# Kernel optimization log

Measured on AMD Instinct MI355X. Metric: run time of the kernel, lower is better.

The kernel has to match this reference:

```python
import jax, jax.numpy as jnp
import numpy as np

B, T, D = 64, 512, 1024
V_TAG, V_TYPE = 6, 20
TAG_PAD, TYPE_PAD = 5, 19
E = 2048          # total entity spans in the batch (sliced cascade mode)
MAX_SPAN = 8      # max entity span length


def setup_inputs() -> dict:
    key = jax.random.key(0)
    ks = jax.random.split(key, 12)
    full_hidden = jax.random.normal(ks[0], (B, T, D), dtype=jnp.float32)
    W_tag = jax.random.normal(ks[1], (D, V_TAG), dtype=jnp.float32) * 0.02
    b_tag = jnp.zeros((V_TAG,), jnp.float32)
    W_type = jax.random.normal(ks[2], (D, V_TYPE), dtype=jnp.float32) * 0.02
    b_type = jnp.zeros((V_TYPE,), jnp.float32)
    crf_start = jax.random.normal(ks[3], (V_TAG,), dtype=jnp.float32) * 0.1
    crf_end = jax.random.normal(ks[4], (V_TAG,), dtype=jnp.float32) * 0.1
    crf_trans = jax.random.normal(ks[5], (V_TAG, V_TAG), dtype=jnp.float32) * 0.1
    # ragged sequence lengths (>= MAX_SPAN+1 so all positions/spans are sane)
    seq_lens = jnp.maximum(jax.random.randint(ks[6], (B,), 1, T + 1), MAX_SPAN + 1).astype(jnp.int32)
    tag_ids = jax.random.randint(ks[7], (B, T), 0, V_TAG - 1).astype(jnp.int32)  # exclude pad tag
    ent_sample_ids = jax.random.randint(ks[8], (E,), 0, B).astype(jnp.int32)
    ent_starts = jax.random.randint(ks[9], (E,), 0, T - MAX_SPAN).astype(jnp.int32)
    ent_lens = jax.random.randint(ks[10], (E,), 1, MAX_SPAN + 1)
    ent_ends = (ent_starts + ent_lens).astype(jnp.int32)
    ent_type_ids = jax.random.randint(ks[11], (E,), 0, V_TYPE - 1).astype(jnp.int32)  # exclude pad type
    return dict(full_hidden=full_hidden, W_tag=W_tag, b_tag=b_tag, W_type=W_type,
                b_type=b_type, crf_start=crf_start, crf_end=crf_end, crf_trans=crf_trans,
                tag_ids=tag_ids, seq_lens=seq_lens, ent_sample_ids=ent_sample_ids,
                ent_starts=ent_starts, ent_ends=ent_ends, ent_type_ids=ent_type_ids)


def reference(full_hidden, W_tag, b_tag, W_type, b_type, crf_start, crf_end, crf_trans,
              tag_ids, seq_lens, ent_sample_ids, ent_starts, ent_ends, ent_type_ids):
    mask = jnp.arange(T)[None, :] < seq_lens[:, None]                  # [B,T] bool (tok_mask)
    maskf = mask.astype(full_hidden.dtype)

    # ---- base CRF decoder: tag projection + CRF NLL per sample ----
    tag_feats = full_hidden @ W_tag + b_tag                            # [B,T,V_TAG]

    # gold path score
    emit_scores = jnp.take_along_axis(tag_feats, tag_ids[..., None].astype(jnp.int32), axis=-1)[..., 0]  # [B,T]
    gold = crf_start[tag_ids[:, 0]] + jnp.sum(emit_scores * maskf, axis=1)
    trans_scores = crf_trans[tag_ids[:, :-1], tag_ids[:, 1:]]          # [B,T-1]
    gold = gold + jnp.sum(trans_scores * maskf[:, 1:], axis=1)
    last_tags = tag_ids[jnp.arange(B), seq_lens - 1]
    gold = gold + crf_end[last_tags]

    # log-partition via forward algorithm (log-sum-exp DP, lax.scan over time)
    alpha0 = crf_start[None, :] + tag_feats[:, 0]                      # [B,V]

    def step(alpha, xs):
        emit_t, mask_t = xs                                            # [B,V], [B]
        new = jax.scipy.special.logsumexp(
            alpha[:, :, None] + crf_trans[None, :, :] + emit_t[:, None, :], axis=1)
        return jnp.where(mask_t[:, None], new, alpha), None

    alphaT, _ = jax.lax.scan(step, alpha0,
                             (jnp.swapaxes(tag_feats, 0, 1)[1:], mask.T[1:]))
    logZ = jax.scipy.special.logsumexp(alphaT + crf_end[None, :], axis=-1)  # [B]
    tag_losses = logZ - gold                                           # per-sample CRF NLL

    # ---- sliced cascade: entity-span mean pooling + CE(sum) per sample ----
    type_feats = full_hidden @ W_type + b_type                         # [B,T,V_TYPE]
    csum = jnp.pad(jnp.cumsum(type_feats, axis=1), ((0, 0), (1, 0), (0, 0)))  # [B,T+1,V_TYPE]
    span_sum = csum[ent_sample_ids, ent_ends] - csum[ent_sample_ids, ent_starts]  # [E,V_TYPE]
    span_len = (ent_ends - ent_starts).astype(type_feats.dtype)
    ent_feats = span_sum / span_len[:, None]                           # mean over span
    logp = jax.nn.log_softmax(ent_feats, axis=-1)
    ent_ce = -jnp.take_along_axis(logp, ent_type_ids[:, None].astype(jnp.int32), axis=-1)[:, 0]
    valid = (ent_type_ids != TYPE_PAD).astype(ent_ce.dtype)            # ignore_index
    type_losses = jax.ops.segment_sum(ent_ce * valid, ent_sample_ids, num_segments=B)
    return tag_losses + type_losses                                    # [B]
```

## Files before the change

kernel.cpp:

```cpp
#include <hip/hip_runtime.h>
#include <math.h>
#include <stdint.h>

#define NB  64
#define NT  512
#define ND  1024
#define NVT 6
#define NVY 20
#define TYPE_PAD_V 19
#define NE  2048
#define LOG2E 1.44269504088896340736f
#define LN2   0.69314718055994530942f

typedef float v2f __attribute__((ext_vector_type(2)));

#define OFF_WTT 196608
#define OFF_CNT 217088
#define OFF_WS2 217104

__global__ __launch_bounds__(256) void k1_tagfeats(const float* __restrict__ H,
                                                   const float* __restrict__ W_tag,
                                                   const float* __restrict__ b_tag,
                                                   const float* __restrict__ W_type,
                                                   float* __restrict__ ws,
                                                   float* __restrict__ out) {
    float* featsT = ws;
    float* WtT    = ws + OFF_WTT;
    if (blockIdx.x == 0) {
        if (threadIdx.x < NB) out[threadIdx.x] = 0.0f;
        if (threadIdx.x == 64) ((int*)(ws + OFF_CNT))[0] = 0;
    }
    if (blockIdx.x < 32) {
        int tid = blockIdx.x * 256 + threadIdx.x;
        for (int i = tid; i < NVY * ND; i += 32 * 256)
            WtT[i] = W_type[(i & (ND - 1)) * NVY + (i >> 10)];
    }

    __shared__ float wlds[NVT][ND];
    for (int i = threadIdx.x; i < ND * NVT; i += 256) {
        int d = i / NVT, v = i % NVT;
        wlds[v][d] = W_tag[i];
    }
    __syncthreads();
    float bt[NVT];
#pragma unroll
    for (int v = 0; v < NVT; ++v) bt[v] = b_tag[v];

    const int lane = threadIdx.x & 63;
    const int wid  = threadIdx.x >> 6;
    const int qw   = lane >> 4;
    const int ql   = lane & 15;
    const int rowBase = blockIdx.x * 32;

#pragma unroll
    for (int it = 0; it < 2; ++it) {
        const int r = rowBase + it * 16 + wid * 4 + qw;
        const float4* hrow = (const float4*)(H + (size_t)r * ND);
        float acc[NVT] = {0.f, 0.f, 0.f, 0.f, 0.f, 0.f};
#pragma unroll
        for (int k = 0; k < 16; ++k) {
            float4 h = hrow[ql + 16 * k];
#pragma unroll
            for (int v = 0; v < NVT; ++v) {
                float4 w = ((const float4*)&wlds[v][0])[ql + 16 * k];
                acc[v] += h.x * w.x + h.y * w.y + h.z * w.z + h.w * w.w;
            }
        }
#pragma unroll
        for (int v = 0; v < NVT; ++v) {
#pragma unroll
            for (int off = 8; off >= 1; off >>= 1)
                acc[v] += __shfl_xor(acc[v], off);
        }
        const int bb = r >> 9;
        const int tt = r & (NT - 1);
#pragma unroll
        for (int v = 0; v < NVT; ++v)
            if (ql == v) featsT[(size_t)tt * 384 + bb * 6 + v] = acc[v] + bt[v];
    }
}

#define LOADC(BUF, c) do {                                                   \
    _Pragma("unroll")                                                        \
    for (int kk = 0; kk < 6; ++kk) {                                         \
        const float4* p = src4 + (size_t)((c) * 6 + kk) * 128;               \
        BUF[2 * kk] = p[0]; BUF[2 * kk + 1] = p[1];                          \
    }                                                                        \
} while (0)

#define CBODY(BUF, c) do {                                                   \
    float i0 = BUF[1].z, i1 = BUF[3].z, i2 = BUF[5].z,                       \
          i3 = BUF[7].z, i4 = BUF[9].z, i5 = BUF[11].z;                      \
    float im = fmaxf(fmaxf(fmaxf(i0, i1), i2), fmaxf(fmaxf(i3, i4), i5));    \
    float w0 = q0 * __builtin_amdgcn_exp2f(i0 - im);                         \
    float w1 = q1 * __builtin_amdgcn_exp2f(i1 - im);                         \
    float w2 = q2 * __builtin_amdgcn_exp2f(i2 - im);                         \
    float w3 = q3 * __builtin_amdgcn_exp2f(i3 - im);                         \
    float w4 = q4 * __builtin_amdgcn_exp2f(i4 - im);                         \
    float w5 = q5 * __builtin_amdgcn_exp2f(i5 - im);                         \
    float n0 = BUF[0].x * w0, n1 = BUF[0].y * w0, n2 = BUF[0].z * w0,        \
          n3 = BUF[0].w * w0, n4 = BUF[1].x * w0, n5 = BUF[1].y * w0;        \
    n0 = __builtin_fmaf(BUF[2].x,  w1, n0); n1 = __builtin_fmaf(BUF[2].y,  w1, n1); \
    n2 = __builtin_fmaf(BUF[2].z,  w1, n2); n3 = __builtin_fmaf(BUF[2].w,  w1, n3); \
    n4 = __builtin_fmaf(BUF[3].x,  w1, n4); n5 = __builtin_fmaf(BUF[3].y,  w1, n5); \
    n0 = __builtin_fmaf(BUF[4].x,  w2, n0); n1 = __builtin_fmaf(BUF[4].y,  w2, n1); \
    n2 = __builtin_fmaf(BUF[4].z,  w2, n2); n3 = __builtin_fmaf(BUF[4].w,  w2, n3); \
    n4 = __builtin_fmaf(BUF[5].x,  w2, n4); n5 = __builtin_fmaf(BUF[5].y,  w2, n5); \
    n0 = __builtin_fmaf(BUF[6].x,  w3, n0); n1 = __builtin_fmaf(BUF[6].y,  w3, n1); \
    n2 = __builtin_fmaf(BUF[6].z,  w3, n2); n3 = __builtin_fmaf(BUF[6].w,  w3, n3); \
    n4 = __builtin_fmaf(BUF[7].x,  w3, n4); n5 = __builtin_fmaf(BUF[7].y,  w3, n5); \
    n0 = __builtin_fmaf(BUF[8].x,  w4, n0); n1 = __builtin_fmaf(BUF[8].y,  w4, n1); \
    n2 = __builtin_fmaf(BUF[8].z,  w4, n2); n3 = __builtin_fmaf(BUF[8].w,  w4, n3); \
    n4 = __builtin_fmaf(BUF[9].x,  w4, n4); n5 = __builtin_fmaf(BUF[9].y,  w4, n5); \
    n0 = __builtin_fmaf(BUF[10].x, w5, n0); n1 = __builtin_fmaf(BUF[10].y, w5, n1); \
    n2 = __builtin_fmaf(BUF[10].z, w5, n2); n3 = __builtin_fmaf(BUF[10].w, w5, n3); \
    n4 = __builtin_fmaf(BUF[11].x, w5, n4); n5 = __builtin_fmaf(BUF[11].y, w5, n5); \
    float qmax = fmaxf(fmaxf(fmaxf(n0, n1), n2), fmaxf(fmaxf(n3, n4), n5));  \
    uint32_t eb = __float_as_uint(qmax) >> 23;                               \
    mAcc2 += (float)((int)eb - 126) + im;                                    \
    float ri = __uint_as_float((uint32_t)(253 - eb) << 23);                  \
    q0 = n0 * ri; q1 = n1 * ri; q2 = n2 * ri;                                \
    q3 = n3 * ri; q4 = n4 * ri; q5 = n5 * ri;                                \
    int lc = (c) + 3; if (lc > 31) lc = 31;                                  \
    LOADC(BUF, lc);                                                          \
} while (0)

__global__ __launch_bounds__(64) void k2_fused(
    const float* __restrict__ H,
    const float* __restrict__ b_type,
    const float* __restrict__ crf_start,
    const float* __restrict__ crf_end,
    const float* __restrict__ crf_trans,
    const int* __restrict__ tag_ids,
    const int* __restrict__ seq_lens,
    const int* __restrict__ ent_sid,
    const int* __restrict__ ent_st,
    const int* __restrict__ ent_en,
    const int* __restrict__ ent_ty,
    float* __restrict__ ws,
    float* __restrict__ out) {
    const float* featsT = ws;
    const float* WtT    = ws + OFF_WTT;
    int* cnt            = (int*)(ws + OFF_CNT);
    float* ws2          = ws + OFF_WS2;
    __shared__ int stag[NT];
    __shared__ float trLp[NVT * NVT];
    __shared__ int isLast;
    const int lane = threadIdx.x;

    if (blockIdx.x < 192) {
        const int c = blockIdx.x / 6;
        const int k = blockIdx.x - 6 * c;
        const int b = lane;
        const int L = seq_lens[b];
        float F[NVT][NVT];
#pragma unroll
        for (int i = 0; i < NVT; ++i)
#pragma unroll
            for (int j = 0; j < NVT; ++j)
                F[i][j] = __builtin_amdgcn_exp2f(crf_trans[i * NVT + j] * LOG2E);
        const char* pf = (const char*)featsT + b * 24;
        v2f Ebuf[16][3];
#pragma unroll
        for (int u = 0; u < 16; ++u) {
            const v2f* p = (const v2f*)(pf + (size_t)(16 * c + 1 + u) * 1536);
            Ebuf[u][0] = p[0]; Ebuf[u][1] = p[1]; Ebuf[u][2] = p[2];
        }
        float v0, v1, v2, v3, v4, v5;
        v0 = (k == 0) ? 1.f : 0.f; v1 = (k == 1) ? 1.f : 0.f; v2 = (k == 2) ? 1.f : 0.f;
        v3 = (k == 3) ? 1.f : 0.f; v4 = (k == 4) ? 1.f : 0.f; v5 = (k == 5) ? 1.f : 0.f;
        int isc = 0;
#pragma unroll
        for (int u = 0; u < 16; ++u) {
            float e0 = __builtin_amdgcn_exp2f(Ebuf[u][0].x * LOG2E);
            float e1 = __builtin_amdgcn_exp2f(Ebuf[u][0].y * LOG2E);
            float e2 = __builtin_amdgcn_exp2f(Ebuf[u][1].x * LOG2E);
            float e3 = __builtin_amdgcn_exp2f(Ebuf[u][1].y * LOG2E);
            float e4 = __builtin_amdgcn_exp2f(Ebuf[u][2].x * LOG2E);
            float e5 = __builtin_amdgcn_exp2f(Ebuf[u][2].y * LOG2E);
            bool ok = (16 * c + 1 + u) < L;
            float g[NVT];
#pragma unroll
            for (int j = 0; j < NVT; ++j) {
                float s = F[0][j] * v0;
                s = __builtin_fmaf(F[1][j], v1, s);
                s = __builtin_fmaf(F[2][j], v2, s);
                s = __builtin_fmaf(F[3][j], v3, s);
                s = __builtin_fmaf(F[4][j], v4, s);
                s = __builtin_fmaf(F[5][j], v5, s);
                g[j] = s;
            }
            v0 = ok ? e0 * g[0] : v0;  v1 = ok ? e1 * g[1] : v1;
            v2 = ok ? e2 * g[2] : v2;  v3 = ok ? e3 * g[3] : v3;
            v4 = ok ? e4 * g[4] : v4;  v5 = ok ? e5 * g[5] : v5;
            if ((u & 3) == 3) {
                float qmax = fmaxf(fmaxf(fmaxf(v0, v1), v2), fmaxf(fmaxf(v3, v4), v5));
                uint32_t eb = __float_as_uint(qmax) >> 23;
                float ri = __uint_as_float((uint32_t)(253 - eb) << 23);
                v0 *= ri; v1 *= ri; v2 *= ri; v3 *= ri; v4 *= ri; v5 *= ri;
                isc += (int)eb - 126;
            }
        }
        float4* dst = (float4*)(ws2 + (((size_t)c * 6 + k) * 64 + b) * 8);
        dst[0] = make_float4(v0, v1, v2, v3);
        dst[1] = make_float4(v4, v5, (float)isc, 0.0f);

        __threadfence();
        if (lane == 0) isLast = (atomicAdd(cnt, 1) == 191);
        __syncthreads();
        if (isLast) {
            __threadfence();
            const int b2 = lane;
            float a0[NVT];
#pragma unroll
            for (int j = 0; j < NVT; ++j) a0[j] = crf_start[j] + featsT[b2 * 6 + j];
            float m0 = fmaxf(fmaxf(fmaxf(a0[0], a0[1]), a0[2]),
                             fmaxf(fmaxf(a0[3], a0[4]), a0[5]));
            float q0 = __builtin_amdgcn_exp2f((a0[0] - m0) * LOG2E);
            float q1 = __builtin_amdgcn_exp2f((a0[1] - m0) * LOG2E);
            float q2 = __builtin_amdgcn_exp2f((a0[2] - m0) * LOG2E);
            float q3 = __builtin_amdgcn_exp2f((a0[3] - m0) * LOG2E);
            float q4 = __builtin_amdgcn_exp2f((a0[4] - m0) * LOG2E);
            float q5 = __builtin_amdgcn_exp2f((a0[5] - m0) * LOG2E);
            float mAcc2 = m0 * LOG2E;

            const float4* src4 = (const float4*)ws2 + b2 * 2;
            float4 PB0[12], PB1[12], PB2[12];
            LOADC(PB0, 0); LOADC(PB1, 1); LOADC(PB2, 2);
#pragma unroll 1
            for (int c0 = 0; c0 < 30; c0 += 3) {
                CBODY(PB0, c0);
                CBODY(PB1, c0 + 1);
                CBODY(PB2, c0 + 2);
            }
            CBODY(PB0, 30);
            CBODY(PB1, 31);

            float zs = q0 * __builtin_amdgcn_exp2f(crf_end[0] * LOG2E)
                     + q1 * __builtin_amdgcn_exp2f(crf_end[1] * LOG2E)
                     + q2 * __builtin_amdgcn_exp2f(crf_end[2] * LOG2E)
                     + q3 * __builtin_amdgcn_exp2f(crf_end[3] * LOG2E)
                     + q4 * __builtin_amdgcn_exp2f(crf_end[4] * LOG2E)
                     + q5 * __builtin_amdgcn_exp2f(crf_end[5] * LOG2E);
            float logZ = LN2 * (mAcc2 + __builtin_amdgcn_logf(zs));
            atomicAdd(&out[b2], logZ);
        }
    } else if (blockIdx.x < 192 + NB) {
        const int b = blockIdx.x - 192;
        for (int i = lane; i < NT; i += 64) stag[i] = tag_ids[b * NT + i];
        if (lane < NVT * NVT) trLp[lane] = crf_trans[lane];
        __syncthreads();
        const int L = seq_lens[b];
        float g = 0.0f;
#pragma unroll
        for (int k = 0; k < NT / 64; ++k) {
            int t = lane + 64 * k;
            if (t < L) {
                int tg = stag[t];
                g += featsT[(size_t)t * 384 + b * 6 + tg];
                if (t >= 1) g += trLp[stag[t - 1] * NVT + tg];
            }
        }
#pragma unroll
        for (int off = 32; off >= 1; off >>= 1) g += __shfl_xor(g, off);
        if (lane == 0)
            atomicAdd(&out[b], -(g + crf_start[stag[0]] + crf_end[stag[L - 1]]));
    } else {
        const int e  = blockIdx.x - 192 - NB;
        const int bb = ent_sid[e];
        const int s  = ent_st[e];
        const int en = ent_en[e];
        const int ty = ent_ty[e];
        float4 sv[4];
#pragma unroll
        for (int k = 0; k < 4; ++k) { sv[k].x = 0.f; sv[k].y = 0.f; sv[k].z = 0.f; sv[k].w = 0.f; }
        for (int t = s; t < en; ++t) {
            const float4* hr = (const float4*)(H + ((size_t)bb * NT + t) * ND);
#pragma unroll
            for (int k = 0; k < 4; ++k) {
                float4 h = hr[lane + 64 * k];
                sv[k].x += h.x; sv[k].y += h.y; sv[k].z += h.z; sv[k].w += h.w;
            }
        }
        const float inv = 1.0f / (float)(en - s);
        float f[NVY];
#pragma unroll
        for (int v = 0; v < NVY; ++v) {
            const float4* wv = (const float4*)(WtT + v * ND);
            float p = 0.0f;
#pragma unroll
            for (int k = 0; k < 4; ++k) {
                float4 w = wv[lane + 64 * k];
                p += sv[k].x * w.x + sv[k].y * w.y + sv[k].z * w.z + sv[k].w * w.w;
            }
#pragma unroll
            for (int off = 32; off >= 1; off >>= 1) p += __shfl_xor(p, off);
            f[v] = p * inv + b_type[v];
        }
        float mx = -3.0e38f;
#pragma unroll
        for (int v = 0; v < NVY; ++v) mx = fmaxf(mx, f[v]);
        float sum = 0.0f, goldf = 0.0f;
#pragma unroll
        for (int v = 0; v < NVY; ++v) {
            sum += __expf(f[v] - mx);
            if (v == ty) goldf = f[v];
        }
        float lse = mx + __logf(sum);
        if (ty != TYPE_PAD_V && lane == 0) atomicAdd(&out[bb], lse - goldf);
    }
}

extern "C" void kernel_launch(void* const* d_in, const int* in_sizes, int n_in,
                              void* d_out, int out_size, void* d_ws, size_t ws_size,
                              hipStream_t stream) {
    const float* H         = (const float*)d_in[0];
    const float* W_tag     = (const float*)d_in[1];
    const float* b_tag     = (const float*)d_in[2];
    const float* W_type    = (const float*)d_in[3];
    const float* b_type    = (const float*)d_in[4];
    const float* crf_start = (const float*)d_in[5];
    const float* crf_end   = (const float*)d_in[6];
    const float* crf_trans = (const float*)d_in[7];
    const int* tag_ids     = (const int*)d_in[8];
    const int* seq_lens    = (const int*)d_in[9];
    const int* ent_sid     = (const int*)d_in[10];
    const int* ent_st      = (const int*)d_in[11];
    const int* ent_en      = (const int*)d_in[12];
    const int* ent_ty      = (const int*)d_in[13];
    float* out = (float*)d_out;
    float* ws  = (float*)d_ws;

    hipLaunchKernelGGL(k1_tagfeats, dim3(1024), dim3(256), 0, stream,
                       H, W_tag, b_tag, W_type, ws, out);
    hipLaunchKernelGGL(k2_fused, dim3(192 + NB + NE), dim3(64), 0, stream,
                       H, b_type, crf_start, crf_end, crf_trans,
                       tag_ids, seq_lens, ent_sid, ent_st, ent_en, ent_ty, ws, out);
}
```

Baseline: 61.44 us.

## Hold tag weights in registers, prefetch rows, and unroll masked span pooling

The tag projection kernel drops the LDS copy of W_tag. Each lane now keeps its own 96 weights in registers, and each wave processes 8 full rows with a one-row-ahead register prefetch and a full-wave shuffle reduction. The entity path replaces its variable-length span loop with a fixed 8-row unrolled loop that masks rows past the span end, so all loads can be issued together. The costs are higher register pressure, loading rows that are masked out, and a wider reduction per row.

```diff
diff --git a/kernel.cpp b/kernel.cpp
--- a/kernel.cpp
+++ b/kernel.cpp
@@ -36,47 +36,80 @@
             WtT[i] = W_type[(i & (ND - 1)) * NVY + (i >> 10)];
     }
 
-    __shared__ float wlds[NVT][ND];
-    for (int i = threadIdx.x; i < ND * NVT; i += 256) {
-        int d = i / NVT, v = i % NVT;
-        wlds[v][d] = W_tag[i];
-    }
-    __syncthreads();
-    float bt[NVT];
-#pragma unroll
-    for (int v = 0; v < NVT; ++v) bt[v] = b_tag[v];
-
     const int lane = threadIdx.x & 63;
-    const int wid  = threadIdx.x >> 6;
-    const int qw   = lane >> 4;
-    const int ql   = lane & 15;
-    const int rowBase = blockIdx.x * 32;
-
-#pragma unroll
-    for (int it = 0; it < 2; ++it) {
-        const int r = rowBase + it * 16 + wid * 4 + qw;
-        const float4* hrow = (const float4*)(H + (size_t)r * ND);
-        float acc[NVT] = {0.f, 0.f, 0.f, 0.f, 0.f, 0.f};
-#pragma unroll
-        for (int k = 0; k < 16; ++k) {
-            float4 h = hrow[ql + 16 * k];
-#pragma unroll
-            for (int v = 0; v < NVT; ++v) {
-                float4 w = ((const float4*)&wlds[v][0])[ql + 16 * k];
-                acc[v] += h.x * w.x + h.y * w.y + h.z * w.z + h.w * w.w;
-            }
-        }
-#pragma unroll
-        for (int v = 0; v < NVT; ++v) {
-#pragma unroll
-            for (int off = 8; off >= 1; off >>= 1)
-                acc[v] += __shfl_xor(acc[v], off);
-        }
-        const int bb = r >> 9;
-        const int tt = r & (NT - 1);
-#pragma unroll
-        for (int v = 0; v < NVT; ++v)
-            if (ql == v) featsT[(size_t)tt * 384 + bb * 6 + v] = acc[v] + bt[v];
+    const int w    = threadIdx.x >> 6;
+    float wk[4][24];
+    const float4* wt4 = (const float4*)W_tag;
+#pragma unroll
+    for (int k = 0; k < 4; ++k) {
+#pragma unroll
+        for (int m = 0; m < 6; ++m) {
+            float4 t = wt4[lane * 6 + k * 384 + m];
+            wk[k][4 * m + 0] = t.x; wk[k][4 * m + 1] = t.y;
+            wk[k][4 * m + 2] = t.z; wk[k][4 * m + 3] = t.w;
+        }
+    }
+    float bt0 = b_tag[0], bt1 = b_tag[1], bt2 = b_tag[2],
+          bt3 = b_tag[3], bt4 = b_tag[4], bt5 = b_tag[5];
+
+    const int rbase = blockIdx.x * 32 + w * 8;
+    const float4* hr = (const float4*)H + (size_t)rbase * 256;
+    float4 h0 = hr[lane], h1 = hr[lane + 64], h2 = hr[lane + 128], h3 = hr[lane + 192];
+#pragma unroll
+    for (int i = 0; i < 8; ++i) {
+        float4 g0, g1, g2, g3;
+        if (i < 7) {
+            const float4* nr = hr + (size_t)(i + 1) * 256;
+            g0 = nr[lane]; g1 = nr[lane + 64]; g2 = nr[lane + 128]; g3 = nr[lane + 192];
+        }
+        float a0 = 0.f, a1 = 0.f, a2 = 0.f, a3 = 0.f, a4 = 0.f, a5 = 0.f;
+#pragma unroll
+        for (int k = 0; k < 4; ++k) {
+            float4 h = (k == 0) ? h0 : (k == 1) ? h1 : (k == 2) ? h2 : h3;
+            a0 = __builtin_fmaf(h.x, wk[k][0],  a0);
+            a1 = __builtin_fmaf(h.x, wk[k][1],  a1);
+            a2 = __builtin_fmaf(h.x, wk[k][2],  a2);
+            a3 = __builtin_fmaf(h.x, wk[k][3],  a3);
+            a4 = __builtin_fmaf(h.x, wk[k][4],  a4);
+            a5 = __builtin_fmaf(h.x, wk[k][5],  a5);
+            a0 = __builtin_fmaf(h.y, wk[k][6],  a0);
+            a1 = __builtin_fmaf(h.y, wk[k][7],  a1);
+            a2 = __builtin_fmaf(h.y, wk[k][8],  a2);
+            a3 = __builtin_fmaf(h.y, wk[k][9],  a3);
+            a4 = __builtin_fmaf(h.y, wk[k][10], a4);
+            a5 = __builtin_fmaf(h.y, wk[k][11], a5);
+            a0 = __builtin_fmaf(h.z, wk[k][12], a0);
+            a1 = __builtin_fmaf(h.z, wk[k][13], a1);
+            a2 = __builtin_fmaf(h.z, wk[k][14], a2);
+            a3 = __builtin_fmaf(h.z, wk[k][15], a3);
+            a4 = __builtin_fmaf(h.z, wk[k][16], a4);
+            a5 = __builtin_fmaf(h.z, wk[k][17], a5);
+            a0 = __builtin_fmaf(h.w, wk[k][18], a0);
+            a1 = __builtin_fmaf(h.w, wk[k][19], a1);
+            a2 = __builtin_fmaf(h.w, wk[k][20], a2);
+            a3 = __builtin_fmaf(h.w, wk[k][21], a3);
+            a4 = __builtin_fmaf(h.w, wk[k][22], a4);
+            a5 = __builtin_fmaf(h.w, wk[k][23], a5);
+        }
+#pragma unroll
+        for (int off = 32; off >= 1; off >>= 1) {
+            a0 += __shfl_xor(a0, off);
+            a1 += __shfl_xor(a1, off);
+            a2 += __shfl_xor(a2, off);
+            a3 += __shfl_xor(a3, off);
+            a4 += __shfl_xor(a4, off);
+            a5 += __shfl_xor(a5, off);
+        }
+        float val = a0 + bt0;
+        val = (lane == 1) ? a1 + bt1 : val;
+        val = (lane == 2) ? a2 + bt2 : val;
+        val = (lane == 3) ? a3 + bt3 : val;
+        val = (lane == 4) ? a4 + bt4 : val;
+        val = (lane == 5) ? a5 + bt5 : val;
+        const int r = rbase + i;
+        if (lane < 6)
+            featsT[(size_t)(r & (NT - 1)) * 384 + (r >> 9) * 6 + lane] = val;
+        h0 = g0; h1 = g1; h2 = g2; h3 = g3;
     }
 }
 
@@ -271,28 +304,37 @@
         const int s  = ent_st[e];
         const int en = ent_en[e];
         const int ty = ent_ty[e];
-        float4 sv[4];
-#pragma unroll
-        for (int k = 0; k < 4; ++k) { sv[k].x = 0.f; sv[k].y = 0.f; sv[k].z = 0.f; sv[k].w = 0.f; }
-        for (int t = s; t < en; ++t) {
-            const float4* hr = (const float4*)(H + ((size_t)bb * NT + t) * ND);
-#pragma unroll
-            for (int k = 0; k < 4; ++k) {
-                float4 h = hr[lane + 64 * k];
-                sv[k].x += h.x; sv[k].y += h.y; sv[k].z += h.z; sv[k].w += h.w;
-            }
+        float4 sv0 = {0,0,0,0}, sv1 = {0,0,0,0}, sv2 = {0,0,0,0}, sv3 = {0,0,0,0};
+        const float4* hb = (const float4*)H + ((size_t)bb * NT + s) * 256;
+#pragma unroll
+        for (int q = 0; q < 8; ++q) {
+            float msk = (s + q < en) ? 1.0f : 0.0f;
+            const float4* hr = hb + (size_t)q * 256;
+            float4 h0 = hr[lane], h1 = hr[lane + 64],
+                   h2 = hr[lane + 128], h3 = hr[lane + 192];
+            sv0.x = __builtin_fmaf(h0.x, msk, sv0.x); sv0.y = __builtin_fmaf(h0.y, msk, sv0.y);
+            sv0.z = __builtin_fmaf(h0.z, msk, sv0.z); sv0.w = __builtin_fmaf(h0.w, msk, sv0.w);
+            sv1.x = __builtin_fmaf(h1.x, msk, sv1.x); sv1.y = __builtin_fmaf(h1.y, msk, sv1.y);
+            sv1.z = __builtin_fmaf(h1.z, msk, sv1.z); sv1.w = __builtin_fmaf(h1.w, msk, sv1.w);
+            sv2.x = __builtin_fmaf(h2.x, msk, sv2.x); sv2.y = __builtin_fmaf(h2.y, msk, sv2.y);
+            sv2.z = __builtin_fmaf(h2.z, msk, sv2.z); sv2.w = __builtin_fmaf(h2.w, msk, sv2.w);
+            sv3.x = __builtin_fmaf(h3.x, msk, sv3.x); sv3.y = __builtin_fmaf(h3.y, msk, sv3.y);
+            sv3.z = __builtin_fmaf(h3.z, msk, sv3.z); sv3.w = __builtin_fmaf(h3.w, msk, sv3.w);
         }
         const float inv = 1.0f / (float)(en - s);
         float f[NVY];
-#pragma unroll
+#pragma unroll 4
         for (int v = 0; v < NVY; ++v) {
             const float4* wv = (const float4*)(WtT + v * ND);
-            float p = 0.0f;
-#pragma unroll
-            for (int k = 0; k < 4; ++k) {
-                float4 w = wv[lane + 64 * k];
-                p += sv[k].x * w.x + sv[k].y * w.y + sv[k].z * w.z + sv[k].w * w.w;
-            }
+            float4 w0 = wv[lane], w1 = wv[lane + 64],
+                   w2 = wv[lane + 128], w3 = wv[lane + 192];
+            float p = sv0.x * w0.x + sv0.y * w0.y + sv0.z * w0.z + sv0.w * w0.w;
+            p = __builtin_fmaf(sv1.x, w1.x, p); p = __builtin_fmaf(sv1.y, w1.y, p);
+            p = __builtin_fmaf(sv1.z, w1.z, p); p = __builtin_fmaf(sv1.w, w1.w, p);
+            p = __builtin_fmaf(sv2.x, w2.x, p); p = __builtin_fmaf(sv2.y, w2.y, p);
+            p = __builtin_fmaf(sv2.z, w2.z, p); p = __builtin_fmaf(sv2.w, w2.w, p);
+            p = __builtin_fmaf(sv3.x, w3.x, p); p = __builtin_fmaf(sv3.y, w3.y, p);
+            p = __builtin_fmaf(sv3.z, w3.z, p); p = __builtin_fmaf(sv3.w, w3.w, p);
 #pragma unroll
             for (int off = 32; off >= 1; off >>= 1) p += __shfl_xor(p, off);
             f[v] = p * inv + b_type[v];
```

Result: slower. 72.02 us (+17.2%).

## Replace last-block atomic combine with a separate deterministic final reduction kernel

Applied to the files above, without the earlier changes.

The last-arriving-block pattern (atomic counter plus threadfence) and the per-entity atomicAdds into the output are removed. Chunk blocks, gold-score blocks and entity blocks now write partial results to workspace, and a new single-block third kernel runs the logZ chain combine, sums entity losses per sample by scanning all entity ids, and writes the output directly. This drops output zeroing and atomic contention and makes the result deterministic, at the cost of an extra kernel launch and a serial single-block tail.

```diff
diff --git a/kernel.cpp b/kernel.cpp
--- a/kernel.cpp
+++ b/kernel.cpp
@@ -15,21 +15,17 @@
 typedef float v2f __attribute__((ext_vector_type(2)));
 
 #define OFF_WTT 196608
-#define OFF_CNT 217088
-#define OFF_WS2 217104
+#define OFF_WS2 217088
+#define OFF_G   315392
+#define OFF_CE  315456
 
 __global__ __launch_bounds__(256) void k1_tagfeats(const float* __restrict__ H,
                                                    const float* __restrict__ W_tag,
                                                    const float* __restrict__ b_tag,
                                                    const float* __restrict__ W_type,
-                                                   float* __restrict__ ws,
-                                                   float* __restrict__ out) {
+                                                   float* __restrict__ ws) {
     float* featsT = ws;
     float* WtT    = ws + OFF_WTT;
-    if (blockIdx.x == 0) {
-        if (threadIdx.x < NB) out[threadIdx.x] = 0.0f;
-        if (threadIdx.x == 64) ((int*)(ws + OFF_CNT))[0] = 0;
-    }
     if (blockIdx.x < 32) {
         int tid = blockIdx.x * 256 + threadIdx.x;
         for (int i = tid; i < NVY * ND; i += 32 * 256)
@@ -77,6 +73,150 @@
 #pragma unroll
         for (int v = 0; v < NVT; ++v)
             if (ql == v) featsT[(size_t)tt * 384 + bb * 6 + v] = acc[v] + bt[v];
+    }
+}
+
+__global__ __launch_bounds__(64) void k2_fused(
+    const float* __restrict__ H,
+    const float* __restrict__ b_type,
+    const float* __restrict__ crf_start,
+    const float* __restrict__ crf_end,
+    const float* __restrict__ crf_trans,
+    const int* __restrict__ tag_ids,
+    const int* __restrict__ seq_lens,
+    const int* __restrict__ ent_sid,
+    const int* __restrict__ ent_st,
+    const int* __restrict__ ent_en,
+    const int* __restrict__ ent_ty,
+    float* __restrict__ ws) {
+    const float* featsT = ws;
+    const float* WtT    = ws + OFF_WTT;
+    float* ws2          = ws + OFF_WS2;
+    float* goldv        = ws + OFF_G;
+    float* cev          = ws + OFF_CE;
+    __shared__ int stag[NT];
+    __shared__ float trLp[NVT * NVT];
+    const int lane = threadIdx.x;
+
+    if (blockIdx.x < 192) {
+        const int c = blockIdx.x / 6;
+        const int k = blockIdx.x - 6 * c;
+        const int b = lane;
+        const int L = seq_lens[b];
+        float F[NVT][NVT];
+#pragma unroll
+        for (int i = 0; i < NVT; ++i)
+#pragma unroll
+            for (int j = 0; j < NVT; ++j)
+                F[i][j] = __builtin_amdgcn_exp2f(crf_trans[i * NVT + j] * LOG2E);
+        const char* pf = (const char*)featsT + b * 24;
+        v2f Ebuf[16][3];
+#pragma unroll
+        for (int u = 0; u < 16; ++u) {
+            const v2f* p = (const v2f*)(pf + (size_t)(16 * c + 1 + u) * 1536);
+            Ebuf[u][0] = p[0]; Ebuf[u][1] = p[1]; Ebuf[u][2] = p[2];
+        }
+        float v0, v1, v2, v3, v4, v5;
+        v0 = (k == 0) ? 1.f : 0.f; v1 = (k == 1) ? 1.f : 0.f; v2 = (k == 2) ? 1.f : 0.f;
+        v3 = (k == 3) ? 1.f : 0.f; v4 = (k == 4) ? 1.f : 0.f; v5 = (k == 5) ? 1.f : 0.f;
+        int isc = 0;
+#pragma unroll
+        for (int u = 0; u < 16; ++u) {
+            float e0 = __builtin_amdgcn_exp2f(Ebuf[u][0].x * LOG2E);
+            float e1 = __builtin_amdgcn_exp2f(Ebuf[u][0].y * LOG2E);
+            float e2 = __builtin_amdgcn_exp2f(Ebuf[u][1].x * LOG2E);
+            float e3 = __builtin_amdgcn_exp2f(Ebuf[u][1].y * LOG2E);
+            float e4 = __builtin_amdgcn_exp2f(Ebuf[u][2].x * LOG2E);
+            float e5 = __builtin_amdgcn_exp2f(Ebuf[u][2].y * LOG2E);
+            bool ok = (16 * c + 1 + u) < L;
+            float g[NVT];
+#pragma unroll
+            for (int j = 0; j < NVT; ++j) {
+                float s = F[0][j] * v0;
+                s = __builtin_fmaf(F[1][j], v1, s);
+                s = __builtin_fmaf(F[2][j], v2, s);
+                s = __builtin_fmaf(F[3][j], v3, s);
+                s = __builtin_fmaf(F[4][j], v4, s);
+                s = __builtin_fmaf(F[5][j], v5, s);
+                g[j] = s;
+            }
+            v0 = ok ? e0 * g[0] : v0;  v1 = ok ? e1 * g[1] : v1;
+            v2 = ok ? e2 * g[2] : v2;  v3 = ok ? e3 * g[3] : v3;
+            v4 = ok ? e4 * g[4] : v4;  v5 = ok ? e5 * g[5] : v5;
+            if ((u & 3) == 3) {
+                float qmax = fmaxf(fmaxf(fmaxf(v0, v1), v2), fmaxf(fmaxf(v3, v4), v5));
+                uint32_t eb = __float_as_uint(qmax) >> 23;
+                float ri = __uint_as_float((uint32_t)(253 - eb) << 23);
+                v0 *= ri; v1 *= ri; v2 *= ri; v3 *= ri; v4 *= ri; v5 *= ri;
+                isc += (int)eb - 126;
+            }
+        }
+        float4* dst = (float4*)(ws2 + (((size_t)c * 6 + k) * 64 + b) * 8);
+        dst[0] = make_float4(v0, v1, v2, v3);
+        dst[1] = make_float4(v4, v5, (float)isc, 0.0f);
+    } else if (blockIdx.x < 192 + NB) {
+        const int b = blockIdx.x - 192;
+        for (int i = lane; i < NT; i += 64) stag[i] = tag_ids[b * NT + i];
+        if (lane < NVT * NVT) trLp[lane] = crf_trans[lane];
+        __syncthreads();
+        const int L = seq_lens[b];
+        float g = 0.0f;
+#pragma unroll
+        for (int k = 0; k < NT / 64; ++k) {
+            int t = lane + 64 * k;
+            if (t < L) {
+                int tg = stag[t];
+                g += featsT[(size_t)t * 384 + b * 6 + tg];
+                if (t >= 1) g += trLp[stag[t - 1] * NVT + tg];
+            }
+        }
+#pragma unroll
+        for (int off = 32; off >= 1; off >>= 1) g += __shfl_xor(g, off);
+        if (lane == 0)
+            goldv[b] = g + crf_start[stag[0]] + crf_end[stag[L - 1]];
+    } else {
+        const int e  = blockIdx.x - 192 - NB;
+        const int bb = ent_sid[e];
+        const int s  = ent_st[e];
+        const int en = ent_en[e];
+        const int ty = ent_ty[e];
+        float4 sv[4];
+#pragma unroll
+        for (int k = 0; k < 4; ++k) { sv[k].x = 0.f; sv[k].y = 0.f; sv[k].z = 0.f; sv[k].w = 0.f; }
+        for (int t = s; t < en; ++t) {
+            const float4* hr = (const float4*)(H + ((size_t)bb * NT + t) * ND);
+#pragma unroll
+            for (int k = 0; k < 4; ++k) {
+                float4 h = hr[lane + 64 * k];
+                sv[k].x += h.x; sv[k].y += h.y; sv[k].z += h.z; sv[k].w += h.w;
+            }
+        }
+        const float inv = 1.0f / (float)(en - s);
+        float f[NVY];
+#pragma unroll
+        for (int v = 0; v < NVY; ++v) {
+            const float4* wv = (const float4*)(WtT + v * ND);
+            float p = 0.0f;
+#pragma unroll
+            for (int k = 0; k < 4; ++k) {
+                float4 w = wv[lane + 64 * k];
+                p += sv[k].x * w.x + sv[k].y * w.y + sv[k].z * w.z + sv[k].w * w.w;
+            }
+#pragma unroll
+            for (int off = 32; off >= 1; off >>= 1) p += __shfl_xor(p, off);
+            f[v] = p * inv + b_type[v];
+        }
+        float mx = -3.0e38f;
+#pragma unroll
+        for (int v = 0; v < NVY; ++v) mx = fmaxf(mx, f[v]);
+        float sum = 0.0f, goldf = 0.0f;
+#pragma unroll
+        for (int v = 0; v < NVY; ++v) {
+            sum += __expf(f[v] - mx);
+            if (v == ty) goldf = f[v];
+        }
+        float lse = mx + __logf(sum);
+        if (lane == 0) cev[e] = (ty != TYPE_PAD_V) ? (lse - goldf) : 0.0f;
     }
 }
 
@@ -125,190 +265,73 @@
     LOADC(BUF, lc);                                                          \
 } while (0)
 
-__global__ __launch_bounds__(64) void k2_fused(
-    const float* __restrict__ H,
-    const float* __restrict__ b_type,
+__global__ __launch_bounds__(128) void k3_final(
     const float* __restrict__ crf_start,
     const float* __restrict__ crf_end,
-    const float* __restrict__ crf_trans,
-    const int* __restrict__ tag_ids,
-    const int* __restrict__ seq_lens,
     const int* __restrict__ ent_sid,
-    const int* __restrict__ ent_st,
-    const int* __restrict__ ent_en,
-    const int* __restrict__ ent_ty,
-    float* __restrict__ ws,
+    const float* __restrict__ ws,
     float* __restrict__ out) {
     const float* featsT = ws;
-    const float* WtT    = ws + OFF_WTT;
-    int* cnt            = (int*)(ws + OFF_CNT);
-    float* ws2          = ws + OFF_WS2;
-    __shared__ int stag[NT];
-    __shared__ float trLp[NVT * NVT];
-    __shared__ int isLast;
-    const int lane = threadIdx.x;
-
-    if (blockIdx.x < 192) {
-        const int c = blockIdx.x / 6;
-        const int k = blockIdx.x - 6 * c;
-        const int b = lane;
-        const int L = seq_lens[b];
-        float F[NVT][NVT];
-#pragma unroll
-        for (int i = 0; i < NVT; ++i)
-#pragma unroll
-            for (int j = 0; j < NVT; ++j)
-                F[i][j] = __builtin_amdgcn_exp2f(crf_trans[i * NVT + j] * LOG2E);
-        const char* pf = (const char*)featsT + b * 24;
-        v2f Ebuf[16][3];
-#pragma unroll
-        for (int u = 0; u < 16; ++u) {
-            const v2f* p = (const v2f*)(pf + (size_t)(16 * c + 1 + u) * 1536);
-            Ebuf[u][0] = p[0]; Ebuf[u][1] = p[1]; Ebuf[u][2] = p[2];
-        }
-        float v0, v1, v2, v3, v4, v5;
-        v0 = (k == 0) ? 1.f : 0.f; v1 = (k == 1) ? 1.f : 0.f; v2 = (k == 2) ? 1.f : 0.f;
-        v3 = (k == 3) ? 1.f : 0.f; v4 = (k == 4) ? 1.f : 0.f; v5 = (k == 5) ? 1.f : 0.f;
-        int isc = 0;
-#pragma unroll
-        for (int u = 0; u < 16; ++u) {
-            float e0 = __builtin_amdgcn_exp2f(Ebuf[u][0].x * LOG2E);
-            float e1 = __builtin_amdgcn_exp2f(Ebuf[u][0].y * LOG2E);
-            float e2 = __builtin_amdgcn_exp2f(Ebuf[u][1].x * LOG2E);
-            float e3 = __builtin_amdgcn_exp2f(Ebuf[u][1].y * LOG2E);
-            float e4 = __builtin_amdgcn_exp2f(Ebuf[u][2].x * LOG2E);
-            float e5 = __builtin_amdgcn_exp2f(Ebuf[u][2].y * LOG2E);
-            bool ok = (16 * c + 1 + u) < L;
-            float g[NVT];
-#pragma unroll
-            for (int j = 0; j < NVT; ++j) {
-                float s = F[0][j] * v0;
-                s = __builtin_fmaf(F[1][j], v1, s);
-                s = __builtin_fmaf(F[2][j], v2, s);
-                s = __builtin_fmaf(F[3][j], v3, s);
-                s = __builtin_fmaf(F[4][j], v4, s);
-                s = __builtin_fmaf(F[5][j], v5, s);
-                g[j] = s;
-            }
-            v0 = ok ? e0 * g[0] : v0;  v1 = ok ? e1 * g[1] : v1;
-            v2 = ok ? e2 * g[2] : v2;  v3 = ok ? e3 * g[3] : v3;
-            v4 = ok ? e4 * g[4] : v4;  v5 = ok ? e5 * g[5] : v5;
-            if ((u & 3) == 3) {
-                float qmax = fmaxf(fmaxf(fmaxf(v0, v1), v2), fmaxf(fmaxf(v3, v4), v5));
-                uint32_t eb = __float_as_uint(qmax) >> 23;
-                float ri = __uint_as_float((uint32_t)(253 - eb) << 23);
-                v0 *= ri; v1 *= ri; v2 *= ri; v3 *= ri; v4 *= ri; v5 *= ri;
-                isc += (int)eb - 126;
-            }
-        }
-        float4* dst = (float4*)(ws2 + (((size_t)c * 6 + k) * 64 + b) * 8);
-        dst[0] = make_float4(v0, v1, v2, v3);
-        dst[1] = make_float4(v4, v5, (float)isc, 0.0f);
-
-        __threadfence();
-        if (lane == 0) isLast = (atomicAdd(cnt, 1) == 191);
-        __syncthreads();
-        if (isLast) {
-            __threadfence();
-            const int b2 = lane;
-            float a0[NVT];
-#pragma unroll
-            for (int j = 0; j < NVT; ++j) a0[j] = crf_start[j] + featsT[b2 * 6 + j];
-            float m0 = fmaxf(fmaxf(fmaxf(a0[0], a0[1]), a0[2]),
-                             fmaxf(fmaxf(a0[3], a0[4]), a0[5]));
-            float q0 = __builtin_amdgcn_exp2f((a0[0] - m0) * LOG2E);
-            float q1 = __builtin_amdgcn_exp2f((a0[1] - m0) * LOG2E);
-            float q2 = __builtin_amdgcn_exp2f((a0[2] - m0) * LOG2E);
-            float q3 = __builtin_amdgcn_exp2f((a0[3] - m0) * LOG2E);
-            float q4 = __builtin_amdgcn_exp2f((a0[4] - m0) * LOG2E);
-            float q5 = __builtin_amdgcn_exp2f((a0[5] - m0) * LOG2E);
-            float mAcc2 = m0 * LOG2E;
-
-            const float4* src4 = (const float4*)ws2 + b2 * 2;
-            float4 PB0[12], PB1[12], PB2[12];
-            LOADC(PB0, 0); LOADC(PB1, 1); LOADC(PB2, 2);
+    const float* ws2    = ws + OFF_WS2;
+    const float* goldv  = ws + OFF_G;
+    const float* cev    = ws + OFF_CE;
+    __shared__ float entSum[NB];
+    const int tid = threadIdx.x;
+
+    if (tid >= 64) {
+        const int b = tid - 64;
+        float acc = 0.0f;
+        const int4* s4 = (const int4*)ent_sid;
+        const float4* c4 = (const float4*)cev;
+        for (int i = 0; i < NE / 4; ++i) {
+            int4 s = s4[i];
+            float4 c = c4[i];
+            acc += (s.x == b) ? c.x : 0.0f;
+            acc += (s.y == b) ? c.y : 0.0f;
+            acc += (s.z == b) ? c.z : 0.0f;
+            acc += (s.w == b) ? c.w : 0.0f;
+        }
+        entSum[b] = acc;
+    }
+    float logZ = 0.0f;
+    if (tid < 64) {
+        const int b2 = tid;
+        float a0[NVT];
+#pragma unroll
+        for (int j = 0; j < NVT; ++j) a0[j] = crf_start[j] + featsT[b2 * 6 + j];
+        float m0 = fmaxf(fmaxf(fmaxf(a0[0], a0[1]), a0[2]),
+                         fmaxf(fmaxf(a0[3], a0[4]), a0[5]));
+        float q0 = __builtin_amdgcn_exp2f((a0[0] - m0) * LOG2E);
+        float q1 = __builtin_amdgcn_exp2f((a0[1] - m0) * LOG2E);
+        float q2 = __builtin_amdgcn_exp2f((a0[2] - m0) * LOG2E);
+        float q3 = __builtin_amdgcn_exp2f((a0[3] - m0) * LOG2E);
+        float q4 = __builtin_amdgcn_exp2f((a0[4] - m0) * LOG2E);
+        float q5 = __builtin_amdgcn_exp2f((a0[5] - m0) * LOG2E);
+        float mAcc2 = m0 * LOG2E;
+
+        const float4* src4 = (const float4*)ws2 + b2 * 2;
+        float4 PB0[12], PB1[12], PB2[12];
+        LOADC(PB0, 0); LOADC(PB1, 1); LOADC(PB2, 2);
 #pragma unroll 1
-            for (int c0 = 0; c0 < 30; c0 += 3) {
-                CBODY(PB0, c0);
-                CBODY(PB1, c0 + 1);
-                CBODY(PB2, c0 + 2);
-            }
-            CBODY(PB0, 30);
-            CBODY(PB1, 31);
-
-            float zs = q0 * __builtin_amdgcn_exp2f(crf_end[0] * LOG2E)
-                     + q1 * __builtin_amdgcn_exp2f(crf_end[1] * LOG2E)
-                     + q2 * __builtin_amdgcn_exp2f(crf_end[2] * LOG2E)
-                     + q3 * __builtin_amdgcn_exp2f(crf_end[3] * LOG2E)
-                     + q4 * __builtin_amdgcn_exp2f(crf_end[4] * LOG2E)
-                     + q5 * __builtin_amdgcn_exp2f(crf_end[5] * LOG2E);
-            float logZ = LN2 * (mAcc2 + __builtin_amdgcn_logf(zs));
-            atomicAdd(&out[b2], logZ);
-        }
-    } else if (blockIdx.x < 192 + NB) {
-        const int b = blockIdx.x - 192;
-        for (int i = lane; i < NT; i += 64) stag[i] = tag_ids[b * NT + i];
-        if (lane < NVT * NVT) trLp[lane] = crf_trans[lane];
-        __syncthreads();
-        const int L = seq_lens[b];
-        float g = 0.0f;
-#pragma unroll
-        for (int k = 0; k < NT / 64; ++k) {
-            int t = lane + 64 * k;
-            if (t < L) {
-                int tg = stag[t];
-                g += featsT[(size_t)t * 384 + b * 6 + tg];
-                if (t >= 1) g += trLp[stag[t - 1] * NVT + tg];
-            }
-        }
-#pragma unroll
-        for (int off = 32; off >= 1; off >>= 1) g += __shfl_xor(g, off);
-        if (lane == 0)
-            atomicAdd(&out[b], -(g + crf_start[stag[0]] + crf_end[stag[L - 1]]));
-    } else {
-        const int e  = blockIdx.x - 192 - NB;
-        const int bb = ent_sid[e];
-        const int s  = ent_st[e];
-        const int en = ent_en[e];
-        const int ty = ent_ty[e];
-        float4 sv[4];
-#pragma unroll
-        for (int k = 0; k < 4; ++k) { sv[k].x = 0.f; sv[k].y = 0.f; sv[k].z = 0.f; sv[k].w = 0.f; }
-        for (int t = s; t < en; ++t) {
-            const float4* hr = (const float4*)(H + ((size_t)bb * NT + t) * ND);
-#pragma unroll
-            for (int k = 0; k < 4; ++k) {
-                float4 h = hr[lane + 64 * k];
-                sv[k].x += h.x; sv[k].y += h.y; sv[k].z += h.z; sv[k].w += h.w;
-            }
-        }
-        const float inv = 1.0f / (float)(en - s);
-        float f[NVY];
-#pragma unroll
-        for (int v = 0; v < NVY; ++v) {
-            const float4* wv = (const float4*)(WtT + v * ND);
-            float p = 0.0f;
-#pragma unroll
-            for (int k = 0; k < 4; ++k) {
-                float4 w = wv[lane + 64 * k];
-                p += sv[k].x * w.x + sv[k].y * w.y + sv[k].z * w.z + sv[k].w * w.w;
-            }
-#pragma unroll
-            for (int off = 32; off >= 1; off >>= 1) p += __shfl_xor(p, off);
-            f[v] = p * inv + b_type[v];
-        }
-        float mx = -3.0e38f;
-#pragma unroll
-        for (int v = 0; v < NVY; ++v) mx = fmaxf(mx, f[v]);
-        float sum = 0.0f, goldf = 0.0f;
-#pragma unroll
-        for (int v = 0; v < NVY; ++v) {
-            sum += __expf(f[v] - mx);
-            if (v == ty) goldf = f[v];
-        }
-        float lse = mx + __logf(sum);
-        if (ty != TYPE_PAD_V && lane == 0) atomicAdd(&out[bb], lse - goldf);
-    }
+        for (int c0 = 0; c0 < 30; c0 += 3) {
+            CBODY(PB0, c0);
+            CBODY(PB1, c0 + 1);
+            CBODY(PB2, c0 + 2);
+        }
+        CBODY(PB0, 30);
+        CBODY(PB1, 31);
+
+        float zs = q0 * __builtin_amdgcn_exp2f(crf_end[0] * LOG2E)
+                 + q1 * __builtin_amdgcn_exp2f(crf_end[1] * LOG2E)
+                 + q2 * __builtin_amdgcn_exp2f(crf_end[2] * LOG2E)
+                 + q3 * __builtin_amdgcn_exp2f(crf_end[3] * LOG2E)
+                 + q4 * __builtin_amdgcn_exp2f(crf_end[4] * LOG2E)
+                 + q5 * __builtin_amdgcn_exp2f(crf_end[5] * LOG2E);
+        logZ = LN2 * (mAcc2 + __builtin_amdgcn_logf(zs));
+    }
+    __syncthreads();
+    if (tid < 64)
+        out[tid] = logZ - goldv[tid] + entSum[tid];
 }
 
 extern "C" void kernel_launch(void* const* d_in, const int* in_sizes, int n_in,
@@ -332,8 +355,10 @@
     float* ws  = (float*)d_ws;
 
     hipLaunchKernelGGL(k1_tagfeats, dim3(1024), dim3(256), 0, stream,
-                       H, W_tag, b_tag, W_type, ws, out);
+                       H, W_tag, b_tag, W_type, ws);
     hipLaunchKernelGGL(k2_fused, dim3(192 + NB + NE), dim3(64), 0, stream,
                        H, b_type, crf_start, crf_end, crf_trans,
-                       tag_ids, seq_lens, ent_sid, ent_st, ent_en, ent_ty, ws, out);
+                       tag_ids, seq_lens, ent_sid, ent_st, ent_en, ent_ty, ws);
+    hipLaunchKernelGGL(k3_final, dim3(1), dim3(128), 0, stream,
+                       crf_start, crf_end, ent_sid, ws, out);
 }
```

Measured after the change: 97.02 us. +57.9%, slower.
